# Optimization experiments

Hardware: AMD Instinct MI355X
Metric: run time of the kernel (lower is better)

## Reference

```python
import jax, jax.numpy as jnp
import numpy as np

G = 8    # deformable groups
K2 = 9   # 3x3 kernel taps


def conv3(x, w, b=None):
    # 3x3, stride 1, SAME padding, NCHW
    y = jax.lax.conv_general_dilated(x, w, (1, 1), 'SAME',
                                     dimension_numbers=('NCHW', 'OIHW', 'NCHW'))
    if b is not None:
        y = y + b[None, :, None, None]
    return y


def deform_conv(x, offset, wgt):
    # DCNv1: x [B,C,H,W], offset [B, G*K2*2, H, W] (per tap: dy,dx), wgt [O,C,3,3]
    B, C, H, W = x.shape
    Cpg = C // G
    off = offset.reshape(B, G, K2, 2, H, W)
    dy, dx = off[:, :, :, 0], off[:, :, :, 1]                      # [B,G,K2,H,W]
    ky = jnp.repeat(jnp.arange(-1, 2), 3).astype(x.dtype)          # tap row offsets
    kx = jnp.tile(jnp.arange(-1, 2), 3).astype(x.dtype)            # tap col offsets
    py = dy + jnp.arange(H, dtype=x.dtype)[None, None, None, :, None] + ky[None, None, :, None, None]
    px = dx + jnp.arange(W, dtype=x.dtype)[None, None, None, None, :] + kx[None, None, :, None, None]
    xg = x.reshape(B, G, Cpg, H * W)
    y0 = jnp.floor(py)
    x0 = jnp.floor(px)

    def corner(yc, xc):
        m = ((yc >= 0) & (yc <= H - 1) & (xc >= 0) & (xc <= W - 1)).astype(x.dtype)
        yi = jnp.clip(yc, 0, H - 1).astype(jnp.int32)
        xi = jnp.clip(xc, 0, W - 1).astype(jnp.int32)
        idx = (yi * W + xi).reshape(B, G, -1)                      # [B,G,K2*H*W]
        v = jax.vmap(jax.vmap(lambda f, i: f[:, i]))(xg, idx)      # [B,G,Cpg,K2*H*W]
        return v.reshape(B, G, Cpg, K2, H, W), m

    v00, m00 = corner(y0, x0)
    v01, m01 = corner(y0, x0 + 1)
    v10, m10 = corner(y0 + 1, x0)
    v11, m11 = corner(y0 + 1, x0 + 1)
    wy = py - y0
    wx = px - x0
    w00 = ((1 - wy) * (1 - wx) * m00)[:, :, None]   # [B,G,1,K2,H,W]
    w01 = ((1 - wy) * wx * m01)[:, :, None]
    w10 = (wy * (1 - wx) * m10)[:, :, None]
    w11 = (wy * wx * m11)[:, :, None]
    sampled = v00 * w00 + v01 * w01 + v10 * w10 + v11 * w11        # [B,G,Cpg,K2,H,W]
    O = wgt.shape[0]
    return jnp.einsum('bgckhw,ogck->bohw', sampled, wgt.reshape(O, G, Cpg, K2))


def setup_inputs() -> dict:
    key = jax.random.key(0)
    ks = jax.random.split(key, 16)

    def he(k, shape):
        # torch init: normal(0, sqrt(2 / (kh*kw*out_ch)))
        o = shape[-4]
        return jax.random.normal(k, shape, jnp.float32) * np.float32(np.sqrt(2.0 / (9 * o)))

    inp = {
        'x': jax.random.normal(ks[0], (2, 5, 3, 128, 128), jnp.float32),
        'conv_first_w': he(ks[1], (64, 3, 3, 3)),
        'conv_first_b': jax.random.normal(ks[2], (64,), jnp.float32) * 0.01,
        'res_w1': he(ks[3], (5, 64, 64, 3, 3)),
        'res_b1': jax.random.normal(ks[4], (5, 64), jnp.float32) * 0.01,
        'res_w2': he(ks[5], (5, 64, 64, 3, 3)),
        'res_b2': jax.random.normal(ks[6], (5, 64), jnp.float32) * 0.01,
        'cr_w': he(ks[7], (64, 128, 3, 3)),
        'cr_b': jax.random.normal(ks[8], (64,), jnp.float32) * 0.01,
        'off_w': he(ks[9], (4, 144, 64, 3, 3)),
        'off_b': jax.random.normal(ks[10], (4, 144), jnp.float32) * 0.01,
        'dconv_w': he(ks[11], (4, 64, 64, 3, 3)),
        'recon_w': he(ks[12], (3, 64, 3, 3)),
        'recon_b': jax.random.normal(ks[13], (3,), jnp.float32) * 0.01,
    }
    return inp


def reference(x, conv_first_w, conv_first_b, res_w1, res_b1, res_w2, res_b2,
              cr_w, cr_b, off_w, off_b, dconv_w, recon_w, recon_b):
    B, N, C, H, W = x.shape
    center = N // 2
    # shared feature trunk over all frames
    out = jax.nn.relu(conv3(x.reshape(B * N, C, H, W), conv_first_w, conv_first_b))
    for i in range(res_w1.shape[0]):
        r = jax.nn.relu(conv3(out, res_w1[i], res_b1[i]))
        out = out + conv3(r, res_w2[i], res_b2[i])
    out = out.reshape(B, N, 64, H, W)
    ref = out[:, center]                                   # [B,64,H,W]
    supp_idx = np.array([i for i in range(N) if i != center])
    supp = out[:, supp_idx].reshape(B * (N - 1), 64, H, W)
    ref_rep = jnp.broadcast_to(ref[:, None], (B, N - 1, 64, H, W)).reshape(B * (N - 1), 64, H, W)
    # alignment cascade (vectorized over the N-1 support frames)
    fea = conv3(jnp.concatenate([ref_rep, supp], axis=1), cr_w, cr_b)
    fea = deform_conv(fea, conv3(fea, off_w[0], off_b[0]), dconv_w[0])
    fea = deform_conv(fea, conv3(fea, off_w[1], off_b[1]), dconv_w[1])
    fea = deform_conv(supp, conv3(fea, off_w[2], off_b[2]), dconv_w[2])
    aligned = deform_conv(fea, conv3(fea, off_w[3], off_b[3]), dconv_w[3])
    im = conv3(aligned, recon_w, recon_b)                  # [B*(N-1),3,H,W]
    ims = im.reshape(B, N - 1, 3, H, W)
    feas = fea.reshape(B, N - 1, 64, H, W)
    x_center = x[:, center]
    lrs = jnp.concatenate([ims[:, :center], x_center[:, None], ims[:, center:]], axis=1)
    feats = jnp.concatenate([feas[:, :center], ref[:, None], feas[:, center:]], axis=1)
    return lrs, feats
```

## Files before the change

### kernel.cpp

```cpp
#include <hip/hip_runtime.h>

#define HH 128
#define WW 128
#define HWX (HH*WW)

using f32x4 = __attribute__((ext_vector_type(4))) float;
using f16x8 = __attribute__((ext_vector_type(8))) _Float16;

__device__ __forceinline__ unsigned short f16bits(_Float16 h) {
  union { _Float16 f; unsigned short u; } v; v.f = h; return v.u;
}
__device__ __forceinline__ _Float16 f16val(unsigned short u) {
  union { unsigned short u; _Float16 f; } v; v.u = u; return v.f;
}

__device__ __forceinline__ int swz(int pos, int q) {
  return pos * 32 + (((q + pos + (pos >> 2)) & 3) << 3);
}

__global__ __launch_bounds__(256) void wprep_k(
    const float* __restrict__ src, unsigned short* __restrict__ dhi,
    unsigned short* __restrict__ dlo, int O, int I, int L)
{
  int idx = blockIdx.x * 256 + threadIdx.x;
  int tot = L * O * I * 9;
  if (idx >= tot) return;
  int per = O * I * 9;
  int layer = idx / per;
  int r = idx - layer * per;
  int o = r / (I * 9);
  int r2 = r - o * (I * 9);
  int i = r2 / 9, k = r2 - i * 9;
  float v = src[idx];
  _Float16 h = (_Float16)v;
  _Float16 l = (_Float16)(v - (float)h);
  long di = (long)layer * per + ((long)k * O + o) * I + i;
  dhi[di] = f16bits(h);
  dlo[di] = f16bits(l);
}

__global__ __launch_bounds__(256) void dwprep_k(
    const float* __restrict__ src, unsigned short* __restrict__ dhi,
    unsigned short* __restrict__ dlo)
{
  int idx = blockIdx.x * 256 + threadIdx.x;
  if (idx >= 147456) return;
  int l = idx / 36864;
  int rem = idx - l * 36864;
  int o = rem / 576;
  int rem2 = rem - o * 576;
  int r = rem2 / 9, k2 = rem2 - r * 9;
  float v = src[idx];
  _Float16 h = (_Float16)v;
  _Float16 lo = (_Float16)(v - (float)h);
  long di = (((long)l * 9 + k2) * 64 + o) * 64 + r;
  dhi[di] = f16bits(h);
  dlo[di] = f16bits(lo);
}

template<int CBLK, int NFRAG, bool RELU, bool ADD, bool CRMODE, int SIN, int SOUT,
         bool ADDSPLIT>
__global__ __launch_bounds__(256, 3) void conv_mfma_k(
    const float* __restrict__ in, const unsigned short* __restrict__ inlo,
    const unsigned short* __restrict__ whi, const unsigned short* __restrict__ wlo,
    const float* __restrict__ bias, const float* __restrict__ res,
    float* __restrict__ out, unsigned short* __restrict__ outh,
    unsigned short* __restrict__ outl,
    int Cout, int nslice, int img_in0, int img_out0)
{
  constexpr int CIN = CBLK * 32;
  constexpr int OCB = NFRAG * 16;
  constexpr int SLAB = OCB * 32;
  __shared__ __align__(16) unsigned short s_in[2 * 10880];
  __shared__ __align__(16) unsigned short s_w[2 * SLAB];

  const int tid = threadIdx.x;
  const int lane = tid & 63;
  const int wv = tid >> 6;
  const int m16 = lane & 15, q = lane >> 4;
  const int iz = blockIdx.z / nslice, slice = blockIdx.z % nslice;
  const int oc_blk0 = slice * OCB;
  const int x0 = blockIdx.x * 32, y0 = blockIdx.y * 8;

  f32x4 acc[4][NFRAG];
#pragma unroll
  for (int mt = 0; mt < 4; ++mt)
#pragma unroll
    for (int nt = 0; nt < NFRAG; ++nt)
#pragma unroll
      for (int i = 0; i < 4; ++i) acc[mt][nt][i] = 0.f;

  int bb = 0, nn = 0;
  const float* inb = in;
  const unsigned short* inb_h = (const unsigned short*)in;
  const unsigned short* inb_l = inlo;
  if (CRMODE) {
    int j = img_in0 + iz;
    bb = j >> 2;
    int ns = j & 3;
    nn = ns < 2 ? ns : ns + 1;
  } else {
    if (SIN == 1) {
      inb_h += (long)(img_in0 + iz) * CIN * HWX;
      inb_l += (long)(img_in0 + iz) * CIN * HWX;
    } else {
      inb = in + (long)(img_in0 + iz) * CIN * HWX;
    }
  }

  for (int cb = 0; cb < CBLK; ++cb) {
    const int c0 = cb * 32;
    if (cb > 0) __syncthreads();
    for (int t = tid; t < 1360; t += 256) {
      int qq = t / 340, pos = t - qq * 340;
      int iy = pos / 34, ix = pos - iy * 34;
      int gy = y0 + iy - 1, gx = x0 + ix - 1;
      bool inr = (gy >= 0 && gy < HH && gx >= 0 && gx < WW);
      if (SIN == 1) {
        uint4 hv = make_uint4(0u, 0u, 0u, 0u), lv = make_uint4(0u, 0u, 0u, 0u);
        if (inr) {
          long a;
          if (CRMODE) {
            int ch = c0 + qq * 8;
            int simg = (ch < 64) ? (bb * 5 + 2) : (bb * 5 + nn);
            a = ((long)(simg * 8 + ((ch & 63) >> 3)) * HWX + gy * WW + gx) * 8;
            hv = *(const uint4*)((const unsigned short*)in + a);
            lv = *(const uint4*)(inlo + a);
          } else {
            a = (long)(c0 + qq * 8) * HWX + (long)(gy * WW + gx) * 8;
            hv = *(const uint4*)(inb_h + a);
            lv = *(const uint4*)(inb_l + a);
          }
        }
        *(uint4*)(s_in + swz(pos, qq)) = hv;
        *(uint4*)(s_in + 10880 + swz(pos, qq)) = lv;
      } else {
        float vals[8];
        if (SIN == 2) {
          if (inr) {
            long a = (long)((c0 >> 3) + qq) * HWX * 8 + (long)(gy * WW + gx) * 8;
            float4 f0 = ((const float4*)(inb + a))[0];
            float4 f1 = ((const float4*)(inb + a))[1];
            vals[0] = f0.x; vals[1] = f0.y; vals[2] = f0.z; vals[3] = f0.w;
            vals[4] = f1.x; vals[5] = f1.y; vals[6] = f1.z; vals[7] = f1.w;
          } else {
#pragma unroll
            for (int j = 0; j < 8; ++j) vals[j] = 0.f;
          }
        } else {
          const float* src;
          if (CRMODE) {
            int ch = c0 + qq * 8;
            int simg = (ch < 64) ? (bb * 5 + 2) : (bb * 5 + nn);
            src = in + ((long)simg * 64 + (ch & 63)) * HWX + gy * WW + gx;
          } else {
            src = inb + (long)(c0 + qq * 8) * HWX + gy * WW + gx;
          }
#pragma unroll
          for (int j = 0; j < 8; ++j)
            vals[j] = inr ? src[(long)j * HWX] : 0.f;
        }
        unsigned hi4[4], lo4[4];
#pragma unroll
        for (int j2 = 0; j2 < 4; ++j2) {
          unsigned short hs[2], ls[2];
#pragma unroll
          for (int j = 0; j < 2; ++j) {
            float v = vals[j2 * 2 + j];
            _Float16 h = (_Float16)v;
            _Float16 l = (_Float16)(v - (float)h);
            hs[j] = f16bits(h); ls[j] = f16bits(l);
          }
          hi4[j2] = (unsigned)hs[0] | ((unsigned)hs[1] << 16);
          lo4[j2] = (unsigned)ls[0] | ((unsigned)ls[1] << 16);
        }
        *(uint4*)(s_in + swz(pos, qq)) = make_uint4(hi4[0], hi4[1], hi4[2], hi4[3]);
        *(uint4*)(s_in + 10880 + swz(pos, qq)) =
            make_uint4(lo4[0], lo4[1], lo4[2], lo4[3]);
      }
    }
    for (int t = tid; t < OCB * 4; t += 256) {
      int qq = t & 3, ocl = t >> 2;
      long so = ((long)0 * Cout + oc_blk0 + ocl) * CIN + c0 + qq * 8;
      *(uint4*)(s_w + swz(ocl, qq)) = *(const uint4*)(whi + so);
      *(uint4*)(s_w + SLAB + swz(ocl, qq)) = *(const uint4*)(wlo + so);
    }
    __syncthreads();

#pragma unroll
    for (int kp = 0; kp < 9; ++kp) {
      uint4 sth, stl;
      int sd = -1;
      if (kp < 8 && tid < OCB * 4) {
        int qq = tid & 3, ocl = tid >> 2;
        long so = ((long)(kp + 1) * Cout + oc_blk0 + ocl) * CIN + c0 + qq * 8;
        sth = *(const uint4*)(whi + so);
        stl = *(const uint4*)(wlo + so);
        sd = swz(ocl, qq);
      }
      const int dy = kp / 3, dx = kp - dy * 3;
      f16x8 bhi[NFRAG], blo[NFRAG];
#pragma unroll
      for (int nt = 0; nt < NFRAG; ++nt) {
        int pw = nt * 16 + m16;
        bhi[nt] = *(const f16x8*)(s_w + swz(pw, q));
        blo[nt] = *(const f16x8*)(s_w + SLAB + swz(pw, q));
      }
#pragma unroll
      for (int mt = 0; mt < 4; ++mt) {
        int r = 2 * wv + (mt >> 1), h = mt & 1;
        int pos = (r + dy) * 34 + h * 16 + m16 + dx;
        f16x8 ahi = *(const f16x8*)(s_in + swz(pos, q));
        f16x8 alo = *(const f16x8*)(s_in + 10880 + swz(pos, q));
#pragma unroll
        for (int nt = 0; nt < NFRAG; ++nt) {
          acc[mt][nt] = __builtin_amdgcn_mfma_f32_16x16x32_f16(
              ahi, blo[nt], acc[mt][nt], 0, 0, 0);
          acc[mt][nt] = __builtin_amdgcn_mfma_f32_16x16x32_f16(
              alo, bhi[nt], acc[mt][nt], 0, 0, 0);
          acc[mt][nt] = __builtin_amdgcn_mfma_f32_16x16x32_f16(
              ahi, bhi[nt], acc[mt][nt], 0, 0, 0);
        }
      }
      if (kp < 8) {
        __syncthreads();
        if (sd >= 0) {
          *(uint4*)(s_w + sd) = sth;
          *(uint4*)(s_w + SLAB + sd) = stl;
        }
        __syncthreads();
      }
    }
  }

  const int img_o = img_out0 + iz;
#pragma unroll
  for (int mt = 0; mt < 4; ++mt) {
    int r = 2 * wv + (mt >> 1), h = mt & 1;
    int y = y0 + r;
    int xb = x0 + h * 16 + q * 4;
#pragma unroll
    for (int nt = 0; nt < NFRAG; ++nt) {
      int oc = oc_blk0 + nt * 16 + m16;
      if (oc < Cout) {
        float bsv = bias[oc];
        long base = ((long)img_o * Cout + oc) * HWX + (long)y * WW + xb;
        long gbase = 0;
        if (SOUT || ADDSPLIT)
          gbase = (long)img_o * Cout * HWX + (long)(oc >> 3) * HWX * 8 +
                  ((long)y * WW + xb) * 8 + (oc & 7);
#pragma unroll
        for (int i = 0; i < 4; ++i) {
          float v = acc[mt][nt][i] + bsv;
          if (RELU) v = fmaxf(v, 0.f);
          if (ADD) {
            if (ADDSPLIT) {
              long gi = gbase + (long)i * 8;
              v += (float)f16val(outh[gi]) + (float)f16val(outl[gi]);
            } else {
              v += res[base + i];
            }
          }
          if (SOUT) {
            _Float16 hh = (_Float16)v;
            outh[gbase + (long)i * 8] = f16bits(hh);
            outl[gbase + (long)i * 8] = f16bits((_Float16)(v - (float)hh));
          }
          if (SOUT != 1) out[base + i] = v;
        }
      }
    }
  }
}

template<int CIN, int CK, int OCB, bool RELU, bool ADD, int SOUT>
__global__ __launch_bounds__(256) void conv3x3_k(
    const float* __restrict__ in, const float* __restrict__ wgt,
    const float* __restrict__ bias, const float* __restrict__ res,
    float* __restrict__ out, unsigned short* __restrict__ outh,
    unsigned short* __restrict__ outl,
    int Cout, int nslice, int img_in0, int img_out0)
{
  __shared__ __align__(16) float s_in[CK][34][34];
  __shared__ __align__(16) float s_w[CK * 9 * OCB];

  const int tid = threadIdx.x;
  const int tx = tid & 31;
  const int ty = tid >> 5;
  const int iz = blockIdx.z / nslice;
  const int slice = blockIdx.z % nslice;
  const int oc0 = slice * OCB;
  const int x0 = blockIdx.x * 32;
  const int y0 = blockIdx.y * 32;

  float acc[4][OCB];
#pragma unroll
  for (int r = 0; r < 4; ++r)
#pragma unroll
    for (int o = 0; o < OCB; ++o) acc[r][o] = 0.f;

  const float* inb = in + (long)(img_in0 + iz) * CIN * HWX;

  for (int c0 = 0; c0 < CIN; c0 += CK) {
    __syncthreads();
    for (int idx = tid; idx < CK * 34 * 34; idx += 256) {
      int c = idx / 1156;
      int rem = idx % 1156;
      int iy = rem / 34, ix = rem % 34;
      int gy = y0 + iy - 1, gx = x0 + ix - 1;
      float v = 0.f;
      if (gy >= 0 && gy < HH && gx >= 0 && gx < WW)
        v = inb[(long)(c0 + c) * HWX + gy * WW + gx];
      s_in[c][iy][ix] = v;
    }
    for (int idx = tid; idx < CK * 9 * OCB; idx += 256) {
      int oc = idx % OCB;
      int ck = idx / OCB;
      int c = ck / 9, k = ck % 9;
      int ocg = oc0 + oc;
      float v = 0.f;
      if (ocg < Cout) v = wgt[((long)ocg * CIN + c0 + c) * 9 + k];
      s_w[idx] = v;
    }
    __syncthreads();

    for (int c = 0; c < CK; ++c) {
#pragma unroll
      for (int k = 0; k < 9; ++k) {
        const int ky = k / 3, kx = k % 3;
        float v0 = s_in[c][ty + ky][tx + kx];
        float v1 = s_in[c][ty + 8 + ky][tx + kx];
        float v2 = s_in[c][ty + 16 + ky][tx + kx];
        float v3 = s_in[c][ty + 24 + ky][tx + kx];
        const float4* wp = (const float4*)&s_w[(c * 9 + k) * OCB];
#pragma unroll
        for (int o4 = 0; o4 < OCB / 4; ++o4) {
          float4 w4 = wp[o4];
          acc[0][o4 * 4 + 0] += v0 * w4.x; acc[0][o4 * 4 + 1] += v0 * w4.y;
          acc[0][o4 * 4 + 2] += v0 * w4.z; acc[0][o4 * 4 + 3] += v0 * w4.w;
          acc[1][o4 * 4 + 0] += v1 * w4.x; acc[1][o4 * 4 + 1] += v1 * w4.y;
          acc[1][o4 * 4 + 2] += v1 * w4.z; acc[1][o4 * 4 + 3] += v1 * w4.w;
          acc[2][o4 * 4 + 0] += v2 * w4.x; acc[2][o4 * 4 + 1] += v2 * w4.y;
          acc[2][o4 * 4 + 2] += v2 * w4.z; acc[2][o4 * 4 + 3] += v2 * w4.w;
          acc[3][o4 * 4 + 0] += v3 * w4.x; acc[3][o4 * 4 + 1] += v3 * w4.y;
          acc[3][o4 * 4 + 2] += v3 * w4.z; acc[3][o4 * 4 + 3] += v3 * w4.w;
        }
      }
    }
  }

#pragma unroll
  for (int o = 0; o < OCB; ++o) {
    int ocg = oc0 + o;
    if (ocg < Cout) {
      float b = bias ? bias[ocg] : 0.f;
      long base = ((long)(img_out0 + iz) * Cout + ocg) * HWX;
#pragma unroll
      for (int r = 0; r < 4; ++r) {
        int y = y0 + ty + 8 * r;
        float v = acc[r][o] + b;
        if (RELU) v = fmaxf(v, 0.f);
        long ia = base + (long)y * WW + x0 + tx;
        if (ADD) v += res[ia];
        if (SOUT) {
          long ga = (long)(img_out0 + iz) * Cout * HWX + (long)(ocg >> 3) * HWX * 8 +
                    ((long)y * WW + x0 + tx) * 8 + (ocg & 7);
          _Float16 hh = (_Float16)v;
          outh[ga] = f16bits(hh);
          outl[ga] = f16bits((_Float16)(v - (float)hh));
        }
        if (SOUT != 1) out[ia] = v;
      }
    }
  }
}

__global__ __launch_bounds__(256) void regroup_k(
    const float* __restrict__ src, float* __restrict__ dst, int supp_mode)
{
  int idx = blockIdx.x * 256 + threadIdx.x;
  int c = idx & 7;
  int p = (idx >> 3) & 16383;
  int g = (idx >> 17) & 7;
  int img = idx >> 20;
  int simg = img;
  if (supp_mode) {
    int b = img >> 2, ns = img & 3;
    simg = b * 5 + (ns < 2 ? ns : ns + 1);
  }
  dst[idx] = src[((simg * 64 + g * 8 + c) * HWX) + p];
}

__global__ __launch_bounds__(256) void deform_mfma_k(
    const float* __restrict__ srcg, const float* __restrict__ off,
    const unsigned short* __restrict__ wh, const unsigned short* __restrict__ wl,
    float* __restrict__ out, int img0, int cmask, int cshift)
{
  __shared__ __align__(16) unsigned short s_w[2][2 * 4096];
  const int tid = threadIdx.x;
  const int lane = tid & 63;
  const int wv = tid >> 6;
  const int m16 = lane & 15, q = lane >> 4;
  const int bid = blockIdx.x;
  const int iz = bid & cmask;
  const int tile = bid >> cshift;
  const int img = img0 + iz;
  const int tp0 = tile * 64;
  const int p = tp0 + wv * 16 + m16;
  const float fy = (float)(p >> 7), fx = (float)(p & 127);
  const int rot = 8 * (m16 & 7);

  const float* offb = off + (long)iz * 144 * HWX + p;
  const float* sgq[2];
  sgq[0] = srcg + (long)(img * 8 + q) * HWX * 8;
  sgq[1] = srcg + (long)(img * 8 + 4 + q) * HWX * 8;

  float dyr[3], dxr[3];
  float pyr[2], pxr[2];
  float4 cr[2][8];

#define LOAD_OFF(T, SLOT) { \
    const float* ob_ = offb + ((long)(4 * ((T) & 1) + q) * 18 + 2 * ((T) >> 1)) * HWX; \
    dyr[SLOT] = ob_[0]; dxr[SLOT] = ob_[HWX]; }

#define ISSUE(T, SLOT, OS) { \
    const int k2_ = (T) >> 1; \
    float py_ = dyr[OS] + fy + (float)(k2_ / 3 - 1); \
    float px_ = dxr[OS] + fx + (float)(k2_ % 3 - 1); \
    pyr[SLOT] = py_; pxr[SLOT] = px_; \
    float y0f_ = floorf(py_), x0f_ = floorf(px_); \
    int yi0_ = (int)fminf(fmaxf(y0f_, 0.f), 127.f); \
    int yi1_ = (int)fminf(fmaxf(y0f_ + 1.f, 0.f), 127.f); \
    int xi0_ = (int)fminf(fmaxf(x0f_, 0.f), 127.f); \
    int xi1_ = (int)fminf(fmaxf(x0f_ + 1.f, 0.f), 127.f); \
    const float* sg_ = sgq[(T) & 1]; \
    const float4* p00_ = (const float4*)(sg_ + ((long)yi0_ * WW + xi0_) * 8); \
    const float4* p01_ = (const float4*)(sg_ + ((long)yi0_ * WW + xi1_) * 8); \
    const float4* p10_ = (const float4*)(sg_ + ((long)yi1_ * WW + xi0_) * 8); \
    const float4* p11_ = (const float4*)(sg_ + ((long)yi1_ * WW + xi1_) * 8); \
    cr[SLOT][0] = p00_[0]; cr[SLOT][1] = p00_[1]; \
    cr[SLOT][2] = p01_[0]; cr[SLOT][3] = p01_[1]; \
    cr[SLOT][4] = p10_[0]; cr[SLOT][5] = p10_[1]; \
    cr[SLOT][6] = p11_[0]; cr[SLOT][7] = p11_[1]; }

#define STAGE(K2) { \
    const int buf_ = (K2) & 1; \
    for (int t2 = tid; t2 < 512; t2 += 256) { \
      int o_ = t2 >> 3, j_ = t2 & 7; \
      int d_ = o_ * 64 + ((8 * j_ + 8 * (o_ & 7)) & 63); \
      long so_ = ((long)(K2) * 64 + o_) * 64 + 8 * j_; \
      *(uint4*)(s_w[buf_] + d_) = *(const uint4*)(wh + so_); \
      *(uint4*)(s_w[buf_] + 4096 + d_) = *(const uint4*)(wl + so_); \
    } }

#define PROCESS(T, SLOT) { \
    float py_ = pyr[SLOT], px_ = pxr[SLOT]; \
    float y0f_ = floorf(py_), x0f_ = floorf(px_); \
    float wy_ = py_ - y0f_, wx_ = px_ - x0f_; \
    float my0 = (y0f_ >= 0.f && y0f_ <= 127.f) ? 1.f : 0.f; \
    float my1 = (y0f_ >= -1.f && y0f_ <= 126.f) ? 1.f : 0.f; \
    float mx0 = (x0f_ >= 0.f && x0f_ <= 127.f) ? 1.f : 0.f; \
    float mx1 = (x0f_ >= -1.f && x0f_ <= 126.f) ? 1.f : 0.f; \
    float w00 = (1.f - wy_) * (1.f - wx_) * my0 * mx0; \
    float w01 = (1.f - wy_) * wx_ * my0 * mx1; \
    float w10 = wy_ * (1.f - wx_) * my1 * mx0; \
    float w11 = wy_ * wx_ * my1 * mx1; \
    f16x8 ah, al; \
    _Pragma("unroll") \
    for (int j = 0; j < 4; ++j) { \
      float v0 = w00 * ((const float*)&cr[SLOT][0])[j] + w01 * ((const float*)&cr[SLOT][2])[j] \
               + w10 * ((const float*)&cr[SLOT][4])[j] + w11 * ((const float*)&cr[SLOT][6])[j]; \
      float v1 = w00 * ((const float*)&cr[SLOT][1])[j] + w01 * ((const float*)&cr[SLOT][3])[j] \
               + w10 * ((const float*)&cr[SLOT][5])[j] + w11 * ((const float*)&cr[SLOT][7])[j]; \
      _Float16 h0 = (_Float16)v0; ah[j] = h0; al[j] = (_Float16)(v0 - (float)h0); \
      _Float16 h1 = (_Float16)v1; ah[4 + j] = h1; al[4 + j] = (_Float16)(v1 - (float)h1); \
    } \
    const unsigned short* wb_ = s_w[((T) >> 1) & 1]; \
    const int roff_ = (32 * ((T) & 1) + 8 * q + rot) & 63; \
    _Pragma("unroll") \
    for (int nt = 0; nt < 4; ++nt) { \
      int o_ = nt * 16 + m16; \
      f16x8 bh = *(const f16x8*)(wb_ + o_ * 64 + roff_); \
      f16x8 bl = *(const f16x8*)(wb_ + 4096 + o_ * 64 + roff_); \
      acc[nt] = __builtin_amdgcn_mfma_f32_16x16x32_f16(ah, bl, acc[nt], 0, 0, 0); \
      acc[nt] = __builtin_amdgcn_mfma_f32_16x16x32_f16(al, bh, acc[nt], 0, 0, 0); \
      acc[nt] = __builtin_amdgcn_mfma_f32_16x16x32_f16(ah, bh, acc[nt], 0, 0, 0); \
    } }

  f32x4 acc[4];
#pragma unroll
  for (int nt = 0; nt < 4; ++nt)
#pragma unroll
    for (int i = 0; i < 4; ++i) acc[nt][i] = 0.f;

  LOAD_OFF(0, 0);
  LOAD_OFF(1, 1);
  ISSUE(0, 0, 0);
  LOAD_OFF(2, 2);
  STAGE(0);
  __syncthreads();

#pragma unroll
  for (int k2 = 0; k2 < 9; ++k2) {
    if (k2 < 8) STAGE(k2 + 1);
#pragma unroll
    for (int s = 0; s < 2; ++s) {
      const int t = 2 * k2 + s;
      if (t < 17) ISSUE(t + 1, (t + 1) & 1, (t + 1) % 3);
      if (t < 15) LOAD_OFF(t + 3, (t + 3) % 3);
      PROCESS(t, t & 1);
    }
    __syncthreads();
  }

#undef LOAD_OFF
#undef ISSUE
#undef STAGE
#undef PROCESS

  const long pb = tp0 + wv * 16 + q * 4;
#pragma unroll
  for (int nt = 0; nt < 4; ++nt) {
    int oc = nt * 16 + m16;
    float4 v;
    v.x = acc[nt][0]; v.y = acc[nt][1]; v.z = acc[nt][2]; v.w = acc[nt][3];
    *(float4*)(out + ((long)img * 64 + oc) * HWX + pb) = v;
  }
}

__global__ __launch_bounds__(256) void assemble_k(
    const float* __restrict__ x, const float* __restrict__ im,
    const float* __restrict__ out0, const float* __restrict__ fea,
    float* __restrict__ out)
{
  int idx = blockIdx.x * 256 + threadIdx.x;
  if (idx < 491520) {
    int within = idx % 49152;
    int n = (idx / 49152) % 5;
    int b = idx / (49152 * 5);
    float v;
    if (n == 2) v = x[(b * 5 + 2) * 49152 + within];
    else {
      int j = b * 4 + (n < 2 ? n : n - 1);
      v = im[j * 49152 + within];
    }
    out[idx] = v;
  } else if (idx < 10977280) {
    int idx2 = idx - 491520;
    int within = idx2 % 1048576;
    int n = (idx2 / 1048576) % 5;
    int b = idx2 / (1048576 * 5);
    float v;
    if (n == 2) v = out0[(b * 5 + 2) * 1048576 + within];
    else {
      int j = b * 4 + (n < 2 ? n : n - 1);
      v = fea[j * 1048576 + within];
    }
    out[idx] = v;
  }
}

extern "C" void kernel_launch(void* const* d_in, const int* in_sizes, int n_in,
                              void* d_out, int out_size, void* d_ws, size_t ws_size,
                              hipStream_t stream) {
  const float* x   = (const float*)d_in[0];
  const float* cfw = (const float*)d_in[1];
  const float* cfb = (const float*)d_in[2];
  const float* rw1 = (const float*)d_in[3];
  const float* rb1 = (const float*)d_in[4];
  const float* rw2 = (const float*)d_in[5];
  const float* rb2 = (const float*)d_in[6];
  const float* crw = (const float*)d_in[7];
  const float* crb = (const float*)d_in[8];
  const float* ofw = (const float*)d_in[9];
  const float* ofb = (const float*)d_in[10];
  const float* dcw = (const float*)d_in[11];
  const float* rcw = (const float*)d_in[12];
  const float* rcb = (const float*)d_in[13];
  float* out = (float*)d_out;

  unsigned short* WH = (unsigned short*)d_ws;
  unsigned short* WL = WH + 774144;
  unsigned short* DH = WH + 1548288;
  unsigned short* DL = DH + 147456;
  const long W_res1 = 0, W_res2 = 184320, W_cr = 368640, W_off = 442368;

  float* A = (float*)d_ws + 921600;
  float* C = A + 10485760;
  float* D = C + 8388608;
  float* F = D + 8388608;
  float* OFF = F + 8388608;
  float* im = D;

  unsigned short* Rh = (unsigned short*)C;
  unsigned short* Rl = Rh + 10485760;
  unsigned short* Ah = (unsigned short*)F;
  unsigned short* Al = Ah + 10485760;

  const size_t fixedF = 921600UL + 10485760UL + 3UL * 8388608UL;
  int chunk = 8;
  while (chunk > 1 && (fixedF + (size_t)chunk * 2359296UL) * sizeof(float) > ws_size)
    chunk >>= 1;
  int cshift = (chunk == 8) ? 3 : (chunk == 4) ? 2 : (chunk == 2) ? 1 : 0;

  dim3 blk(256);

  wprep_k<<<720, blk, 0, stream>>>(rw1, WH + W_res1, WL + W_res1, 64, 64, 5);
  wprep_k<<<720, blk, 0, stream>>>(rw2, WH + W_res2, WL + W_res2, 64, 64, 5);
  wprep_k<<<288, blk, 0, stream>>>(crw, WH + W_cr, WL + W_cr, 64, 128, 1);
  wprep_k<<<1296, blk, 0, stream>>>(ofw, WH + W_off, WL + W_off, 144, 64, 4);
  dwprep_k<<<576, blk, 0, stream>>>(dcw, DH, DL);

  conv3x3_k<3, 3, 16, true, false, 1><<<dim3(4, 4, 40), blk, 0, stream>>>(
      x, cfw, cfb, nullptr, A, Ah, Al, 64, 4, 0, 0);

  for (int i = 0; i < 5; ++i) {
    conv_mfma_k<2, 4, true, false, false, 1, 1, false>
        <<<dim3(4, 16, 10), blk, 0, stream>>>(
        (const float*)Ah, Al, WH + W_res1 + (long)i * 36864, WL + W_res1 + (long)i * 36864,
        rb1 + i * 64, nullptr, A, Rh, Rl, 64, 1, 0, 0);
    if (i < 4)
      conv_mfma_k<2, 4, false, true, false, 1, 1, true>
          <<<dim3(4, 16, 10), blk, 0, stream>>>(
          (const float*)Rh, Rl, WH + W_res2 + (long)i * 36864, WL + W_res2 + (long)i * 36864,
          rb2 + i * 64, nullptr, A, Ah, Al, 64, 1, 0, 0);
    else
      conv_mfma_k<2, 4, false, true, false, 1, 2, true>
          <<<dim3(4, 16, 10), blk, 0, stream>>>(
          (const float*)Rh, Rl, WH + W_res2 + (long)i * 36864, WL + W_res2 + (long)i * 36864,
          rb2 + i * 64, nullptr, A, Ah, Al, 64, 1, 0, 0);
  }

  conv_mfma_k<4, 4, false, false, true, 1, 0, false>
      <<<dim3(4, 16, 8), blk, 0, stream>>>(
      (const float*)Ah, Al, WH + W_cr, WL + W_cr, crb, nullptr, C, nullptr, nullptr,
      64, 1, 0, 0);

  auto off_deform = [&](const float* fea_in, const float* grouped,
                        int layer, float* outp, bool gin) {
    for (int i0 = 0; i0 < 8; i0 += chunk) {
      if (gin)
        conv_mfma_k<2, 3, false, false, false, 2, 0, false>
            <<<dim3(4, 16, chunk * 3), blk, 0, stream>>>(
                grouped, nullptr, WH + W_off + (long)layer * 82944,
                WL + W_off + (long)layer * 82944, ofb + layer * 144,
                nullptr, OFF, nullptr, nullptr, 144, 3, i0, 0);
      else
        conv_mfma_k<2, 3, false, false, false, 0, 0, false>
            <<<dim3(4, 16, chunk * 3), blk, 0, stream>>>(
                fea_in, nullptr, WH + W_off + (long)layer * 82944,
                WL + W_off + (long)layer * 82944, ofb + layer * 144,
                nullptr, OFF, nullptr, nullptr, 144, 3, i0, 0);
      deform_mfma_k<<<dim3(256 * chunk), blk, 0, stream>>>(
          grouped, OFF, DH + (long)layer * 36864, DL + (long)layer * 36864,
          outp, i0, chunk - 1, cshift);
    }
  };

  regroup_k<<<32768, blk, 0, stream>>>(C, D, 0);
  off_deform(C, D, 0, C, true);

  regroup_k<<<32768, blk, 0, stream>>>(C, D, 0);
  off_deform(C, D, 1, C, true);

  regroup_k<<<32768, blk, 0, stream>>>(A, D, 1);
  off_deform(C, D, 2, F, false);

  regroup_k<<<32768, blk, 0, stream>>>(F, D, 0);
  off_deform(F, D, 3, C, true);

  conv3x3_k<64, 8, 4, false, false, 0><<<dim3(4, 4, 8), blk, 0, stream>>>(
      C, rcw, rcb, nullptr, im, nullptr, nullptr, 3, 1, 0, 0);

  assemble_k<<<42880, blk, 0, stream>>>(x, im, A, F, out);
}
```

Measured before the change: 1.696 ms.

## Register-prefetch next channel block of conv input tile during MFMA compute

For the packed-fp16 and fp32-grouped input layouts, the halo tile for the next 32-channel block is now loaded into registers before the current block's MFMA loop and written to LDS at the start of the next iteration. Each wave handles one 8-channel quarter, and lanes step over the 340 positions. The goal is to hide global-load latency behind compute instead of stalling at each block boundary. The cost is many more live registers (up to 6 uint4 pairs or 12 float4), which can lower occupancy or cause spills.

```diff
diff --git a/kernel.cpp b/kernel.cpp
--- a/kernel.cpp
+++ b/kernel.cpp
@@ -108,57 +108,99 @@
     }
   }
 
+  uint4 ph[6], pl[6];
+  float4 pg[6][2];
+
+#define PREFETCH(CBN) do { \
+    const int c0p = (CBN) * 32; \
+    _Pragma("unroll") \
+    for (int r = 0; r < 6; ++r) { \
+      int pos = lane + 64 * r; \
+      int iy = pos / 34, ix = pos - iy * 34; \
+      int gy = y0 + iy - 1, gx = x0 + ix - 1; \
+      bool ok = (pos < 340) && (gy >= 0 && gy < HH && gx >= 0 && gx < WW); \
+      if (SIN == 1) { \
+        ph[r] = make_uint4(0u, 0u, 0u, 0u); pl[r] = make_uint4(0u, 0u, 0u, 0u); \
+        if (ok) { \
+          long a; \
+          if (CRMODE) { \
+            int ch = c0p + wv * 8; \
+            int simg = (ch < 64) ? (bb * 5 + 2) : (bb * 5 + nn); \
+            a = ((long)(simg * 8 + ((ch & 63) >> 3)) * HWX + gy * WW + gx) * 8; \
+            ph[r] = *(const uint4*)((const unsigned short*)in + a); \
+            pl[r] = *(const uint4*)(inlo + a); \
+          } else { \
+            a = (long)(c0p + wv * 8) * HWX + (long)(gy * WW + gx) * 8; \
+            ph[r] = *(const uint4*)(inb_h + a); \
+            pl[r] = *(const uint4*)(inb_l + a); \
+          } \
+        } \
+      } else if (SIN == 2) { \
+        pg[r][0] = make_float4(0.f, 0.f, 0.f, 0.f); \
+        pg[r][1] = make_float4(0.f, 0.f, 0.f, 0.f); \
+        if (ok) { \
+          long a = (long)((c0p >> 3) + wv) * HWX * 8 + (long)(gy * WW + gx) * 8; \
+          pg[r][0] = ((const float4*)(inb + a))[0]; \
+          pg[r][1] = ((const float4*)(inb + a))[1]; \
+        } \
+      } \
+    } \
+  } while (0)
+
+  if (SIN == 1 || SIN == 2) PREFETCH(0);
+
   for (int cb = 0; cb < CBLK; ++cb) {
     const int c0 = cb * 32;
     if (cb > 0) __syncthreads();
-    for (int t = tid; t < 1360; t += 256) {
-      int qq = t / 340, pos = t - qq * 340;
-      int iy = pos / 34, ix = pos - iy * 34;
-      int gy = y0 + iy - 1, gx = x0 + ix - 1;
-      bool inr = (gy >= 0 && gy < HH && gx >= 0 && gx < WW);
-      if (SIN == 1) {
-        uint4 hv = make_uint4(0u, 0u, 0u, 0u), lv = make_uint4(0u, 0u, 0u, 0u);
-        if (inr) {
-          long a;
-          if (CRMODE) {
-            int ch = c0 + qq * 8;
-            int simg = (ch < 64) ? (bb * 5 + 2) : (bb * 5 + nn);
-            a = ((long)(simg * 8 + ((ch & 63) >> 3)) * HWX + gy * WW + gx) * 8;
-            hv = *(const uint4*)((const unsigned short*)in + a);
-            lv = *(const uint4*)(inlo + a);
+    if (SIN == 1 || SIN == 2) {
+#pragma unroll
+      for (int r = 0; r < 6; ++r) {
+        int pos = lane + 64 * r;
+        if (pos < 340) {
+          if (SIN == 1) {
+            *(uint4*)(s_in + swz(pos, wv)) = ph[r];
+            *(uint4*)(s_in + 10880 + swz(pos, wv)) = pl[r];
           } else {
-            a = (long)(c0 + qq * 8) * HWX + (long)(gy * WW + gx) * 8;
-            hv = *(const uint4*)(inb_h + a);
-            lv = *(const uint4*)(inb_l + a);
+            float vals[8];
+            vals[0] = pg[r][0].x; vals[1] = pg[r][0].y;
+            vals[2] = pg[r][0].z; vals[3] = pg[r][0].w;
+            vals[4] = pg[r][1].x; vals[5] = pg[r][1].y;
+            vals[6] = pg[r][1].z; vals[7] = pg[r][1].w;
+            unsigned hi4[4], lo4[4];
+#pragma unroll
+            for (int j2 = 0; j2 < 4; ++j2) {
+              unsigned short hs[2], ls[2];
+#pragma unroll
+              for (int j = 0; j < 2; ++j) {
+                float v = vals[j2 * 2 + j];
+                _Float16 h = (_Float16)v;
+                _Float16 l = (_Float16)(v - (float)h);
+                hs[j] = f16bits(h); ls[j] = f16bits(l);
+              }
+              hi4[j2] = (unsigned)hs[0] | ((unsigned)hs[1] << 16);
+              lo4[j2] = (unsigned)ls[0] | ((unsigned)ls[1] << 16);
+            }
+            *(uint4*)(s_in + swz(pos, wv)) =
+                make_uint4(hi4[0], hi4[1], hi4[2], hi4[3]);
+            *(uint4*)(s_in + 10880 + swz(pos, wv)) =
+                make_uint4(lo4[0], lo4[1], lo4[2], lo4[3]);
           }
         }
-        *(uint4*)(s_in + swz(pos, qq)) = hv;
-        *(uint4*)(s_in + 10880 + swz(pos, qq)) = lv;
-      } else {
-        float vals[8];
-        if (SIN == 2) {
-          if (inr) {
-            long a = (long)((c0 >> 3) + qq) * HWX * 8 + (long)(gy * WW + gx) * 8;
-            float4 f0 = ((const float4*)(inb + a))[0];
-            float4 f1 = ((const float4*)(inb + a))[1];
-            vals[0] = f0.x; vals[1] = f0.y; vals[2] = f0.z; vals[3] = f0.w;
-            vals[4] = f1.x; vals[5] = f1.y; vals[6] = f1.z; vals[7] = f1.w;
-          } else {
-#pragma unroll
-            for (int j = 0; j < 8; ++j) vals[j] = 0.f;
-          }
+      }
+      if (cb + 1 < CBLK) PREFETCH(cb + 1);
+    } else {
+      for (int t = tid; t < 1360; t += 256) {
+        int qq = t / 340, pos = t - qq * 340;
+        int iy = pos / 34, ix = pos - iy * 34;
+        int gy = y0 + iy - 1, gx = x0 + ix - 1;
+        bool inr = (gy >= 0 && gy < HH && gx >= 0 && gx < WW);
+        const float* src;
+        if (CRMODE) {
+          int ch = c0 + qq * 8;
+          int simg = (ch < 64) ? (bb * 5 + 2) : (bb * 5 + nn);
+          src = in + ((long)simg * 64 + (ch & 63)) * HWX + gy * WW + gx;
         } else {
-          const float* src;
-          if (CRMODE) {
-            int ch = c0 + qq * 8;
-            int simg = (ch < 64) ? (bb * 5 + 2) : (bb * 5 + nn);
-            src = in + ((long)simg * 64 + (ch & 63)) * HWX + gy * WW + gx;
-          } else {
-            src = inb + (long)(c0 + qq * 8) * HWX + gy * WW + gx;
-          }
-#pragma unroll
-          for (int j = 0; j < 8; ++j)
-            vals[j] = inr ? src[(long)j * HWX] : 0.f;
+          src = inb + (long)(c0 + qq * 8) * HWX + gy * WW + gx;
         }
         unsigned hi4[4], lo4[4];
 #pragma unroll
@@ -166,7 +208,7 @@
           unsigned short hs[2], ls[2];
 #pragma unroll
           for (int j = 0; j < 2; ++j) {
-            float v = vals[j2 * 2 + j];
+            float v = inr ? src[(long)(j2 * 2 + j) * HWX] : 0.f;
             _Float16 h = (_Float16)v;
             _Float16 l = (_Float16)(v - (float)h);
             hs[j] = f16bits(h); ls[j] = f16bits(l);
@@ -232,6 +274,7 @@
       }
     }
   }
+#undef PREFETCH
 
   const int img_o = img_out0 + iz;
 #pragma unroll
```

Result: slower. 2.133 ms (+25.8%).
